# Kernel optimization log

Hardware: AMD Instinct MI355X
Metric: run time of the kernel (lower is better)

Reference implementation:

```python
import jax, jax.numpy as jnp
import numpy as np

B, S, D = 4, 2048, 1024


def setup_inputs() -> dict:
    key = jax.random.key(0)
    kx, kq, kk, kv, km = jax.random.split(key, 5)
    x = jax.random.normal(kx, (B, S, D), dtype=jnp.float32)
    # bias-free Linear weights, torch convention W: (out, in), y = x @ W.T
    Wq = jax.random.normal(kq, (D, D), dtype=jnp.float32) * 0.02
    Wk = jax.random.normal(kk, (D, D), dtype=jnp.float32) * 0.02
    Wv = jax.random.normal(kv, (D, D), dtype=jnp.float32) * 0.02
    # quantum mask: probability vector per batch over seq positions
    q_mask = jax.nn.softmax(jax.random.normal(km, (B, S), dtype=jnp.float32), axis=-1)
    return {"x": x, "Wq": Wq, "Wk": Wk, "Wv": Wv, "q_mask": q_mask}


def reference(x, Wq, Wk, Wv, q_mask):
    # projections (torch Linear: x @ W.T)
    q = jnp.einsum("bsd,ed->bse", x, Wq)
    k = jnp.einsum("bsd,ed->bse", x, Wk)
    v = jnp.einsum("bsd,ed->bse", x, Wv)
    scale = 1.0 / jnp.sqrt(jnp.asarray(D, dtype=x.dtype))
    scores = jnp.einsum("bqe,bke->bqk", q, k) * scale  # (B, S, S)
    # per-row multiplicative quantum mask (mask broadcast over key dim)
    scores = scores * q_mask[:, :, None]
    attn = jax.nn.softmax(scores, axis=-1)
    out = jnp.einsum("bqk,bkd->bqd", attn, v)
    return out
```

## Files before the change

kernel.cpp:

```cpp
#include <hip/hip_runtime.h>
#include <hip/hip_bf16.h>

#define BB 4
#define SS 2048
#define DD 1024

using f32x4  = __attribute__((ext_vector_type(4))) float;
using i32x4  = __attribute__((ext_vector_type(4))) int;
using i32x8  = __attribute__((ext_vector_type(8))) int;

struct f8_t { unsigned char b; };

__device__ __forceinline__ void gld16(const void* g, void* l) {
    __builtin_amdgcn_global_load_lds(
        (const __attribute__((address_space(1))) void*)(g),
        (__attribute__((address_space(3))) void*)(l),
        16, 0, 0);
}

__device__ __forceinline__ void store1(float* p, float v) { *p = v; }
__device__ __forceinline__ void store1(f8_t* p, float v)  {
    p->b = (unsigned char)(__builtin_amdgcn_cvt_pk_fp8_f32(v, v, 0, false) & 0xff);
}

__global__ void cvt_x_kernel(const float* __restrict__ x, unsigned char* __restrict__ x8, int n8) {
    int i = blockIdx.x * blockDim.x + threadIdx.x;
    if (i >= n8) return;
    float4 a = ((const float4*)x)[2 * i];
    float4 b = ((const float4*)x)[2 * i + 1];
    int lo = __builtin_amdgcn_cvt_pk_fp8_f32(a.x, a.y, 0, false);
    lo     = __builtin_amdgcn_cvt_pk_fp8_f32(a.z, a.w, lo, true);
    int hi = __builtin_amdgcn_cvt_pk_fp8_f32(b.x, b.y, 0, false);
    hi     = __builtin_amdgcn_cvt_pk_fp8_f32(b.z, b.w, hi, true);
    ((int2*)x8)[i] = make_int2(lo, hi);
}

__global__ void cvt_w_kernel(const float* __restrict__ Wq, const float* __restrict__ Wk,
                             const float* __restrict__ Wv, unsigned char* __restrict__ w8, int n8) {
    int i = blockIdx.x * blockDim.x + threadIdx.x;
    int seg = i / n8;
    int j = i - seg * n8;
    const float* src = (seg == 0) ? Wq : (seg == 1) ? Wk : Wv;
    float4 a = ((const float4*)src)[2 * j];
    float4 b = ((const float4*)src)[2 * j + 1];
    int lo = __builtin_amdgcn_cvt_pk_fp8_f32(a.x, a.y, 0, false);
    lo     = __builtin_amdgcn_cvt_pk_fp8_f32(a.z, a.w, lo, true);
    int hi = __builtin_amdgcn_cvt_pk_fp8_f32(b.x, b.y, 0, false);
    hi     = __builtin_amdgcn_cvt_pk_fp8_f32(b.z, b.w, hi, true);
    ((int2*)(w8 + (size_t)seg * n8 * 8))[j] = make_int2(lo, hi);
}

__global__ void xsum_kernel(const float* __restrict__ x, float* __restrict__ xsum) {
    int bd = blockIdx.x;
    int b  = bd >> 2, dc = bd & 3;
    int d  = dc * 256 + threadIdx.x;
    int s0 = blockIdx.y * 128;
    const float* p = x + ((size_t)b * SS + s0) * DD + d;
    float acc = 0.f;
    for (int i = 0; i < 128; ++i) acc += p[(size_t)i * DD];
    atomicAdd(&xsum[b * DD + d], acc);
}

__global__ void colsumv_kernel(const float* __restrict__ Wv, const float* __restrict__ xsum,
                               float* __restrict__ colsum) {
    int idx  = blockIdx.x * 4 + (threadIdx.x >> 6);
    int b    = idx >> 10, c = idx & 1023;
    int lane = threadIdx.x & 63;
    const float* wr = Wv + (size_t)c * DD;
    const float* xs = xsum + b * DD;
    float acc = 0.f;
#pragma unroll 4
    for (int d = lane; d < DD; d += 64) acc += wr[d] * xs[d];
#pragma unroll
    for (int off = 32; off; off >>= 1) acc += __shfl_xor(acc, off);
    if (lane == 0) colsum[idx] = acc;
}

template <int MODE, typename CT>
__global__ __launch_bounds__(512, 2) void gemm_f8(
    const unsigned char* __restrict__ A, const unsigned char* __restrict__ B,
    CT* __restrict__ C, int M, int N, int K,
    long batchA, long batchB, long batchC,
    int ldc, int col_shift, long cstride,
    const float* __restrict__ qmask, float* __restrict__ rsum,
    const float* __restrict__ colsum) {
    constexpr int BM = 256, BN = 128, BK = 128;
    constexpr int SCALE_A = (MODE == 3) ? 118 : 127;
    __shared__ __attribute__((aligned(16))) unsigned char As[2][BM * BK];
    __shared__ __attribute__((aligned(16))) unsigned char Bs[2][BN * BK];

    const int tid  = threadIdx.x;
    const int lane = tid & 63;
    const int wv   = tid >> 6;
    const int l16  = lane & 15;
    const int quad = lane >> 4;
    const int wm   = wv >> 1;
    const int wn   = wv & 1;

    const int m0 = blockIdx.y * BM;
    const int n0 = blockIdx.x * BN;
    const long z = blockIdx.z;
    const unsigned char* Ab = A + z * batchA;
    const unsigned char* Bb = B + z * batchB;

    const int cbase = 2 * quad;

    f32x4 acc[4][4] = {};

#define STAGE_A(buf, kt, j) do {                                              \
        int slot_ = (j) * 512 + tid;                                          \
        int r_ = slot_ >> 3;                                                  \
        int c_ = (slot_ & 7) ^ (r_ & 7);                                      \
        gld16(Ab + (size_t)(m0 + r_) * K + ((kt) + c_ * 16),                  \
              &As[buf][((j) * 512 + wv * 64) * 16]);                          \
    } while (0)
#define STAGE_B(buf, kt, j) do {                                              \
        int slot_ = (j) * 512 + tid;                                          \
        int r_ = slot_ >> 3;                                                  \
        int c_ = (slot_ & 7) ^ (r_ & 7);                                      \
        gld16(Bb + (size_t)(n0 + r_) * K + ((kt) + c_ * 16),                  \
              &Bs[buf][((j) * 512 + wv * 64) * 16]);                          \
    } while (0)
#define RDFRAG(f, base, r) do {                                               \
        int cc_ = cbase ^ ((r) & 7);                                          \
        i32x4 p0_ = *(const i32x4*)((base) + (r) * 128 + cc_ * 16);           \
        i32x4 p1_ = *(const i32x4*)((base) + (r) * 128 + (cc_ ^ 1) * 16);     \
        f[0]=p0_[0]; f[1]=p0_[1]; f[2]=p0_[2]; f[3]=p0_[3];                   \
        f[4]=p1_[0]; f[5]=p1_[1]; f[6]=p1_[2]; f[7]=p1_[3];                   \
    } while (0)
#define MFMA(d, a, b) \
        d = __builtin_amdgcn_mfma_scale_f32_16x16x128_f8f6f4(a, b, d, 0, 0, 0, SCALE_A, 0, 127)

    STAGE_A(0, 0, 0); STAGE_A(0, 0, 1); STAGE_A(0, 0, 2); STAGE_A(0, 0, 3);
    STAGE_B(0, 0, 0); STAGE_B(0, 0, 1);
    asm volatile("s_waitcnt vmcnt(0)" ::: "memory");
    __builtin_amdgcn_s_barrier();

    const int NT = K / BK;
    for (int t = 0; t < NT; ++t) {
        const int cur = t & 1;
        const int nxt = cur ^ 1;
        const unsigned char* Ac = &As[cur][0];
        const unsigned char* Bc = &Bs[cur][0];
        const int ktn = (t + 1) * BK;
        const bool pf = (t + 1 < NT);

        i32x8 a0, a1, a2, a3, b0, b1, b2, b3;

        RDFRAG(a0, Ac, wm * 64 +  0 + l16);
        RDFRAG(a1, Ac, wm * 64 + 16 + l16);
        RDFRAG(b0, Bc, wn * 64 +  0 + l16);
        RDFRAG(b1, Bc, wn * 64 + 16 + l16);
        if (pf) { STAGE_A(nxt, ktn, 0); STAGE_A(nxt, ktn, 1); STAGE_A(nxt, ktn, 2); }
        __builtin_amdgcn_s_barrier();
        asm volatile("s_waitcnt lgkmcnt(0)" ::: "memory");
        __builtin_amdgcn_sched_barrier(0);
        __builtin_amdgcn_s_setprio(1);
        MFMA(acc[0][0], a0, b0); MFMA(acc[0][1], a0, b1);
        MFMA(acc[1][0], a1, b0); MFMA(acc[1][1], a1, b1);
        __builtin_amdgcn_s_setprio(0);
        __builtin_amdgcn_s_barrier();

        RDFRAG(b2, Bc, wn * 64 + 32 + l16);
        RDFRAG(b3, Bc, wn * 64 + 48 + l16);
        if (pf) { STAGE_A(nxt, ktn, 3); STAGE_B(nxt, ktn, 0); STAGE_B(nxt, ktn, 1); }
        __builtin_amdgcn_s_barrier();
        asm volatile("s_waitcnt lgkmcnt(0)" ::: "memory");
        __builtin_amdgcn_sched_barrier(0);
        __builtin_amdgcn_s_setprio(1);
        MFMA(acc[0][2], a0, b2); MFMA(acc[0][3], a0, b3);
        MFMA(acc[1][2], a1, b2); MFMA(acc[1][3], a1, b3);
        __builtin_amdgcn_s_setprio(0);
        __builtin_amdgcn_s_barrier();

        RDFRAG(a2, Ac, wm * 64 + 32 + l16);
        RDFRAG(a3, Ac, wm * 64 + 48 + l16);
        __builtin_amdgcn_s_barrier();
        asm volatile("s_waitcnt lgkmcnt(0)" ::: "memory");
        __builtin_amdgcn_sched_barrier(0);
        __builtin_amdgcn_s_setprio(1);
        MFMA(acc[2][2], a2, b2); MFMA(acc[2][3], a2, b3);
        MFMA(acc[3][2], a3, b2); MFMA(acc[3][3], a3, b3);
        MFMA(acc[2][0], a2, b0); MFMA(acc[2][1], a2, b1);
        MFMA(acc[3][0], a3, b0); MFMA(acc[3][1], a3, b1);
        __builtin_amdgcn_s_setprio(0);
        asm volatile("s_waitcnt vmcnt(0)" ::: "memory");
        __builtin_amdgcn_s_barrier();
    }
#undef STAGE_A
#undef STAGE_B
#undef RDFRAG
#undef MFMA

    CT* Cb = C + z * batchC;

    if constexpr (MODE == 0) {
#pragma unroll
        for (int mi = 0; mi < 4; ++mi)
#pragma unroll
            for (int ni = 0; ni < 4; ++ni) {
                int colg = n0 + wn * 64 + ni * 16 + l16;
#pragma unroll
                for (int r = 0; r < 4; ++r) {
                    int rowg = m0 + wm * 64 + mi * 16 + quad * 4 + r;
                    store1(Cb + (size_t)rowg * ldc + colg, acc[mi][ni][r]);
                }
            }
    } else if constexpr (MODE == 1) {
#pragma unroll
        for (int mi = 0; mi < 4; ++mi)
#pragma unroll
            for (int ni = 0; ni < 4; ++ni) {
                int colg = n0 + wn * 64 + ni * 16 + l16;
                int cb   = colg >> col_shift;
                int ccol = colg - (cb << col_shift);
#pragma unroll
                for (int r = 0; r < 4; ++r) {
                    int rowg = m0 + wm * 64 + mi * 16 + quad * 4 + r;
                    store1(Cb + (long)cb * cstride + (size_t)rowg * ldc + ccol, acc[mi][ni][r]);
                }
            }
    } else if constexpr (MODE == 2) {
        const float* qm = qmask + (z << 11);
        float* rs = rsum + (z << 11);
#pragma unroll
        for (int mi = 0; mi < 4; ++mi) {
#pragma unroll
            for (int r = 0; r < 4; ++r) {
                int rowg = m0 + wm * 64 + mi * 16 + quad * 4 + r;
                float fac = qm[rowg] * 0.03125f;
                float part = 0.f;
#pragma unroll
                for (int ni = 0; ni < 4; ++ni) {
                    int colg = n0 + wn * 64 + ni * 16 + l16;
                    float t = __expf(acc[mi][ni][r] * fac) - 1.0f;
                    part += t;
                    store1(Cb + (size_t)rowg * ldc + colg, t * 512.0f);
                }
                part += __shfl_xor(part, 1);
                part += __shfl_xor(part, 2);
                part += __shfl_xor(part, 4);
                part += __shfl_xor(part, 8);
                if (l16 == 0) atomicAdd(&rs[rowg], part);
            }
        }
    } else {
        const float* rs = rsum + (z << 11);
        const float* cs = colsum + (z << 10);
#pragma unroll
        for (int mi = 0; mi < 4; ++mi) {
#pragma unroll
            for (int r = 0; r < 4; ++r) {
                int rowg = m0 + wm * 64 + mi * 16 + quad * 4 + r;
                float inv = 1.0f / (2048.0f + rs[rowg]);
#pragma unroll
                for (int ni = 0; ni < 4; ++ni) {
                    int colg = n0 + wn * 64 + ni * 16 + l16;
                    store1(Cb + (size_t)rowg * ldc + colg, (acc[mi][ni][r] + cs[colg]) * inv);
                }
            }
        }
    }
}

extern "C" void kernel_launch(void* const* d_in, const int* in_sizes, int n_in,
                              void* d_out, int out_size, void* d_ws, size_t ws_size,
                              hipStream_t stream) {
    const float* x     = (const float*)d_in[0];
    const float* Wq    = (const float*)d_in[1];
    const float* Wk    = (const float*)d_in[2];
    const float* Wv    = (const float*)d_in[3];
    const float* qmask = (const float*)d_in[4];
    float* out = (float*)d_out;

    const long nx = (long)BB * SS * DD;
    const long nw = (long)DD * DD;

    unsigned char* ws  = (unsigned char*)d_ws;
    unsigned char* x8  = ws;
    unsigned char* w8  = x8 + nx;
    unsigned char* qk8 = w8 + 3 * nw;
    unsigned char* vt8 = qk8 + 2 * nx;
    unsigned char* t8  = vt8 + nx;
    float* xsum   = (float*)(t8 + (long)BB * SS * SS);
    float* rs     = xsum + BB * DD;
    float* colsum = rs + BB * SS;

    hipMemsetAsync(xsum, 0, (size_t)(BB * DD + BB * SS) * sizeof(float), stream);

    cvt_x_kernel<<<dim3((int)(nx / 8 / 256)), dim3(256), 0, stream>>>(x, x8, (int)(nx / 8));
    cvt_w_kernel<<<dim3((int)(3 * nw / 8 / 256)), dim3(256), 0, stream>>>(Wq, Wk, Wv, w8, (int)(nw / 8));
    xsum_kernel<<<dim3(16, 16), dim3(256), 0, stream>>>(x, xsum);
    colsumv_kernel<<<dim3(1024), dim3(256), 0, stream>>>(Wv, xsum, colsum);

    gemm_f8<0, f8_t><<<dim3(DD / 128, (BB * SS) / 256, 2), 512, 0, stream>>>(
        x8, w8, (f8_t*)qk8, BB * SS, DD, DD, 0, nw, nx, DD, 31, 0, nullptr, nullptr, nullptr);

    gemm_f8<1, f8_t><<<dim3((BB * SS) / 128, DD / 256, 1), 512, 0, stream>>>(
        w8 + 2 * nw, x8, (f8_t*)vt8, DD, BB * SS, DD, 0, 0, 0, SS, 11, (long)DD * SS,
        nullptr, nullptr, nullptr);

    gemm_f8<2, f8_t><<<dim3(SS / 128, SS / 256, BB), 512, 0, stream>>>(
        qk8, qk8 + nx, (f8_t*)t8, SS, SS, DD, (long)SS * DD, (long)SS * DD, (long)SS * SS,
        SS, 31, 0, qmask, rs, nullptr);

    gemm_f8<3, float><<<dim3(DD / 128, SS / 256, BB), 512, 0, stream>>>(
        t8, vt8, out, SS, DD, SS, (long)SS * SS, (long)DD * SS, (long)SS * DD,
        DD, 31, 0, nullptr, rs, colsum);
}
```

Before: 230.2 us.

## Triple-buffer FP8 GEMM K-loop and swizzle workgroups across XCDs

The FP8 MFMA GEMM's LDS double buffer becomes a three-stage ring. Each iteration prefetches tile t+2 up front, then waits with vmcnt(6), so only the older stage has to land before the single end-of-iteration barrier. The three intra-iteration barriers and lgkmcnt waits go away, and all 16 MFMAs run in one priority-raised block. Workgroup IDs are also remapped in groups of 8 so blocks landing on the same XCD share A/B tiles in L2. The cost is more LDS per block (144KB), and the remap assumes the workgroup count is a multiple of 8.

```diff
diff --git a/kernel.cpp b/kernel.cpp
--- a/kernel.cpp
+++ b/kernel.cpp
@@ -86,8 +86,8 @@
     const float* __restrict__ colsum) {
     constexpr int BM = 256, BN = 128, BK = 128;
     constexpr int SCALE_A = (MODE == 3) ? 118 : 127;
-    __shared__ __attribute__((aligned(16))) unsigned char As[2][BM * BK];
-    __shared__ __attribute__((aligned(16))) unsigned char Bs[2][BN * BK];
+    __shared__ __attribute__((aligned(16))) unsigned char As[3][BM * BK];
+    __shared__ __attribute__((aligned(16))) unsigned char Bs[3][BN * BK];
 
     const int tid  = threadIdx.x;
     const int lane = tid & 63;
@@ -97,8 +97,13 @@
     const int wm   = wv >> 1;
     const int wn   = wv & 1;
 
-    const int m0 = blockIdx.y * BM;
-    const int n0 = blockIdx.x * BN;
+    const int gx  = gridDim.x;
+    const int nwg = gx * gridDim.y;
+    const int lin = blockIdx.y * gx + blockIdx.x;
+    const int cpx = nwg >> 3;
+    const int swz = (lin & 7) * cpx + (lin >> 3);
+    const int m0 = (swz / gx) * BM;
+    const int n0 = (swz % gx) * BN;
     const long z = blockIdx.z;
     const unsigned char* Ab = A + z * batchA;
     const unsigned char* Bb = B + z * batchB;
@@ -133,59 +138,51 @@
 
     STAGE_A(0, 0, 0); STAGE_A(0, 0, 1); STAGE_A(0, 0, 2); STAGE_A(0, 0, 3);
     STAGE_B(0, 0, 0); STAGE_B(0, 0, 1);
-    asm volatile("s_waitcnt vmcnt(0)" ::: "memory");
+    STAGE_A(1, BK, 0); STAGE_A(1, BK, 1); STAGE_A(1, BK, 2); STAGE_A(1, BK, 3);
+    STAGE_B(1, BK, 0); STAGE_B(1, BK, 1);
+    asm volatile("s_waitcnt vmcnt(6)" ::: "memory");
     __builtin_amdgcn_s_barrier();
+    __builtin_amdgcn_sched_barrier(0);
 
     const int NT = K / BK;
+    int cur = 0;
     for (int t = 0; t < NT; ++t) {
-        const int cur = t & 1;
-        const int nxt = cur ^ 1;
         const unsigned char* Ac = &As[cur][0];
         const unsigned char* Bc = &Bs[cur][0];
-        const int ktn = (t + 1) * BK;
-        const bool pf = (t + 1 < NT);
-
+
+        if (t + 2 < NT) {
+            int nb = cur + 2; if (nb >= 3) nb -= 3;
+            int ktn = (t + 2) * BK;
+            STAGE_A(nb, ktn, 0); STAGE_A(nb, ktn, 1);
+            STAGE_A(nb, ktn, 2); STAGE_A(nb, ktn, 3);
+            STAGE_B(nb, ktn, 0); STAGE_B(nb, ktn, 1);
+        }
+
+        __builtin_amdgcn_s_setprio(1);
         i32x8 a0, a1, a2, a3, b0, b1, b2, b3;
-
+        RDFRAG(b0, Bc, wn * 64 +  0 + l16);
+        RDFRAG(b1, Bc, wn * 64 + 16 + l16);
+        RDFRAG(b2, Bc, wn * 64 + 32 + l16);
+        RDFRAG(b3, Bc, wn * 64 + 48 + l16);
         RDFRAG(a0, Ac, wm * 64 +  0 + l16);
         RDFRAG(a1, Ac, wm * 64 + 16 + l16);
-        RDFRAG(b0, Bc, wn * 64 +  0 + l16);
-        RDFRAG(b1, Bc, wn * 64 + 16 + l16);
-        if (pf) { STAGE_A(nxt, ktn, 0); STAGE_A(nxt, ktn, 1); STAGE_A(nxt, ktn, 2); }
-        __builtin_amdgcn_s_barrier();
-        asm volatile("s_waitcnt lgkmcnt(0)" ::: "memory");
-        __builtin_amdgcn_sched_barrier(0);
-        __builtin_amdgcn_s_setprio(1);
         MFMA(acc[0][0], a0, b0); MFMA(acc[0][1], a0, b1);
+        MFMA(acc[0][2], a0, b2); MFMA(acc[0][3], a0, b3);
         MFMA(acc[1][0], a1, b0); MFMA(acc[1][1], a1, b1);
-        __builtin_amdgcn_s_setprio(0);
-        __builtin_amdgcn_s_barrier();
-
-        RDFRAG(b2, Bc, wn * 64 + 32 + l16);
-        RDFRAG(b3, Bc, wn * 64 + 48 + l16);
-        if (pf) { STAGE_A(nxt, ktn, 3); STAGE_B(nxt, ktn, 0); STAGE_B(nxt, ktn, 1); }
-        __builtin_amdgcn_s_barrier();
-        asm volatile("s_waitcnt lgkmcnt(0)" ::: "memory");
-        __builtin_amdgcn_sched_barrier(0);
-        __builtin_amdgcn_s_setprio(1);
-        MFMA(acc[0][2], a0, b2); MFMA(acc[0][3], a0, b3);
         MFMA(acc[1][2], a1, b2); MFMA(acc[1][3], a1, b3);
-        __builtin_amdgcn_s_setprio(0);
-        __builtin_amdgcn_s_barrier();
-
         RDFRAG(a2, Ac, wm * 64 + 32 + l16);
         RDFRAG(a3, Ac, wm * 64 + 48 + l16);
+        MFMA(acc[2][0], a2, b0); MFMA(acc[2][1], a2, b1);
+        MFMA(acc[2][2], a2, b2); MFMA(acc[2][3], a2, b3);
+        MFMA(acc[3][0], a3, b0); MFMA(acc[3][1], a3, b1);
+        MFMA(acc[3][2], a3, b2); MFMA(acc[3][3], a3, b3);
+        __builtin_amdgcn_s_setprio(0);
+
+        if (t + 2 < NT) asm volatile("s_waitcnt vmcnt(6)" ::: "memory");
+        else            asm volatile("s_waitcnt vmcnt(0)" ::: "memory");
         __builtin_amdgcn_s_barrier();
-        asm volatile("s_waitcnt lgkmcnt(0)" ::: "memory");
         __builtin_amdgcn_sched_barrier(0);
-        __builtin_amdgcn_s_setprio(1);
-        MFMA(acc[2][2], a2, b2); MFMA(acc[2][3], a2, b3);
-        MFMA(acc[3][2], a3, b2); MFMA(acc[3][3], a3, b3);
-        MFMA(acc[2][0], a2, b0); MFMA(acc[2][1], a2, b1);
-        MFMA(acc[3][0], a3, b0); MFMA(acc[3][1], a3, b1);
-        __builtin_amdgcn_s_setprio(0);
-        asm volatile("s_waitcnt vmcnt(0)" ::: "memory");
-        __builtin_amdgcn_s_barrier();
+        if (++cur == 3) cur = 0;
     }
 #undef STAGE_A
 #undef STAGE_B
```

Result: faster. 221.3 us (-3.9%).
